# Kernel tuning notes

Measured on AMD Instinct MI355X. Metric: run time of the kernel, lower is better.

Reference implementation:

```python
import jax, jax.numpy as jnp
import numpy as np

B, L, D, H, DH, DL, NB = 8, 1024, 512, 8, 64, 64, 128
EPS = 1e-6


def layer_norm(x, g, b):
    m = jnp.mean(x, axis=-1, keepdims=True)
    v = jnp.mean((x - m) ** 2, axis=-1, keepdims=True)
    return (x - m) * jax.lax.rsqrt(v + EPS) * g + b


def rel_bias(timestamps, pos_w, ts_w):
    # position part: skew trick, pos_w has length 2L-1
    t = jnp.concatenate([pos_w, jnp.zeros((L,), pos_w.dtype)])  # (3L-1,)
    t = jnp.tile(t, L)[:-L].reshape(L, 3 * L - 2)
    rel_pos = t[:, L - 1:2 * L - 1]  # (L, L)
    # timestamp part: bucketized pairwise diffs of extended timestamps
    ext = jnp.concatenate([timestamps, timestamps[:, L - 1:L]], axis=1)  # (B, L+1)
    d = ext[:, 1:, None] - ext[:, None, :-1]  # (B, L, L)
    mag = jnp.maximum(jnp.abs(d).astype(jnp.float32), 1.0)
    bucket = jnp.clip((jnp.log(mag) / 0.301).astype(jnp.int32), 0, NB)
    rel_ts = ts_w[bucket]  # (B, L, L)
    return rel_pos[None] + rel_ts


def setup_inputs() -> dict:
    key = jax.random.key(0)
    ks = jax.random.split(key, 8)
    x = jax.random.normal(ks[0], (B, L, D), dtype=jnp.float32)
    timestamps = jnp.sort(jax.random.randint(ks[1], (B, L), 0, 1000000, dtype=jnp.int64), axis=1)
    attn_mask = jnp.triu(jnp.ones((L, L), jnp.float32), k=1)[None, None]  # 1 = masked (future)
    total_out = 2 * DL * H + 2 * DH * H
    uvqk_w = jax.random.normal(ks[2], (D, total_out), dtype=jnp.float32) * 0.02
    out_w = jax.random.normal(ks[3], (DL * H, D), dtype=jnp.float32) * 0.02
    out_b = jnp.zeros((D,), jnp.float32)
    ln1_g = jnp.ones((D,), jnp.float32); ln1_b = jnp.zeros((D,), jnp.float32)
    ln2_g = jnp.ones((DL * H,), jnp.float32); ln2_b = jnp.zeros((DL * H,), jnp.float32)
    ts_weights = jax.random.normal(ks[4], (NB + 1,), dtype=jnp.float32) * 0.02
    pos_weights = jax.random.normal(ks[5], (2 * L - 1,), dtype=jnp.float32) * 0.02
    return {"x": x, "timestamps": timestamps, "attn_mask": attn_mask,
            "uvqk_w": uvqk_w, "out_w": out_w, "out_b": out_b,
            "ln1_g": ln1_g, "ln1_b": ln1_b, "ln2_g": ln2_g, "ln2_b": ln2_b,
            "ts_weights": ts_weights, "pos_weights": pos_weights}


def reference(x, timestamps, attn_mask, uvqk_w, out_w, out_b,
              ln1_g, ln1_b, ln2_g, ln2_b, ts_weights, pos_weights):
    z = layer_norm(x, ln1_g, ln1_b)
    z = jax.nn.silu(z @ uvqk_w)  # linear_activation == 'silu'
    u, v, q, k = jnp.split(z, [DL * H, 2 * DL * H, 2 * DL * H + DH * H], axis=-1)
    q = q.reshape(B, L, H, DH)
    k = k.reshape(B, L, H, DH)
    v = v.reshape(B, L, H, DL)
    scores = jnp.einsum('bmhd,bnhd->bhmn', q, k)
    scores = scores + rel_bias(timestamps, pos_weights, ts_weights)[:, None]
    scores = jax.nn.silu(scores) / L * (1.0 - attn_mask)
    z = jnp.einsum('bhmn,bnhd->bmhd', scores, v).reshape(B, L, H * DL)
    z = layer_norm(z, ln2_g, ln2_b) * u  # gated LN
    return z @ out_w + out_b + x
```

## Files before the change

### kernel.cpp

```cpp
#include <hip/hip_runtime.h>
#include <math.h>

constexpr int Bc = 8;
constexpr int Lc = 1024;
constexpr int Dc = 512;
constexpr int Hc = 8;
constexpr int DHc = 64;
constexpr int DLc = 64;
constexpr int NBc = 128;
constexpr int TOTAL_OUT = 2 * DLc * Hc + 2 * DHc * Hc;
constexpr int ROWS = Bc * Lc;

using f32x4 = __attribute__((ext_vector_type(4))) float;
using s16x8 = __attribute__((ext_vector_type(8))) short;

__device__ __forceinline__ float bf2f(ushort u) {
    union { unsigned int i; float f; } v; v.i = ((unsigned int)u) << 16; return v.f;
}
__device__ __forceinline__ ushort f2bf(float f) {
    union { float f; unsigned int i; } v; v.f = f;
    unsigned int r = v.i + 0x7fffu + ((v.i >> 16) & 1u);
    return (ushort)(r >> 16);
}
__device__ __forceinline__ unsigned int cvtpk_bf16(float lo, float hi) {
    unsigned int r;
    asm("v_cvt_pk_bf16_f32 %0, %1, %2" : "=v"(r) : "v"(lo), "v"(hi));
    return r;
}
__device__ __forceinline__ float silu(float x) {
    float e = __expf(-x);
    return x * __builtin_amdgcn_rcpf(1.0f + e);
}

__global__ __launch_bounds__(256) void transpose_cast(const float* __restrict__ in,
                                                      ushort* __restrict__ out,
                                                      int R, int C) {
    __shared__ float tile[32][33];
    int bc = blockIdx.x * 32, br = blockIdx.y * 32;
    int tx = threadIdx.x & 31, ty = threadIdx.x >> 5;
    for (int i = ty; i < 32; i += 8) {
        int r = br + i, c = bc + tx;
        tile[i][tx] = (r < R && c < C) ? in[(size_t)r * C + c] : 0.f;
    }
    __syncthreads();
    for (int i = ty; i < 32; i += 8) {
        int c = bc + i, r = br + tx;
        if (c < C && r < R) out[(size_t)c * R + r] = f2bf(tile[tx][i]);
    }
}

__global__ __launch_bounds__(256) void ln1_kernel(const float* __restrict__ x,
                                                  const float* __restrict__ g,
                                                  const float* __restrict__ bta,
                                                  ushort* __restrict__ outp) {
    int wid = threadIdx.x >> 6, lane = threadIdx.x & 63;
    int row = blockIdx.x * 4 + wid;
    const float4* xr = (const float4*)(x + (size_t)row * Dc);
    float4 a = xr[lane * 2], c = xr[lane * 2 + 1];
    float xv[8] = {a.x, a.y, a.z, a.w, c.x, c.y, c.z, c.w};
    float s = 0.f, q = 0.f;
#pragma unroll
    for (int i = 0; i < 8; i++) { s += xv[i]; q += xv[i] * xv[i]; }
#pragma unroll
    for (int off = 32; off; off >>= 1) { s += __shfl_xor(s, off); q += __shfl_xor(q, off); }
    float mean = s * (1.f / 512.f);
    float var  = q * (1.f / 512.f) - mean * mean;
    float rstd = rsqrtf(var + 1e-6f);
    const float4* gv = (const float4*)g; const float4* bv = (const float4*)bta;
    float4 g0 = gv[lane * 2], g1 = gv[lane * 2 + 1];
    float4 b0 = bv[lane * 2], b1 = bv[lane * 2 + 1];
    float G[8] = {g0.x, g0.y, g0.z, g0.w, g1.x, g1.y, g1.z, g1.w};
    float Bv[8] = {b0.x, b0.y, b0.z, b0.w, b1.x, b1.y, b1.z, b1.w};
    union { ushort u16[8]; uint4 v; } pk;
#pragma unroll
    for (int i = 0; i < 8; i++) pk.u16[i] = f2bf((xv[i] - mean) * rstd * G[i] + Bv[i]);
    ((uint4*)(outp + (size_t)row * Dc))[lane] = pk.v;
}

__global__ __launch_bounds__(256) void bias_kernel(const int* __restrict__ ts,
                                                   const float* __restrict__ pos_w,
                                                   const float* __restrict__ ts_w,
                                                   ushort* __restrict__ biasb) {
    __shared__ float posw[2 * Lc - 1];
    __shared__ float tsw[NBc + 1];
    int tid = threadIdx.x;
    int b = blockIdx.y;
    for (int i = tid; i < 2 * Lc - 1; i += 256) posw[i] = pos_w[i];
    if (tid < NBc + 1) tsw[tid] = ts_w[tid];
    __syncthreads();
    int m = blockIdx.x * 8 + (tid >> 5);
    int n0 = (tid & 31) * 32;
    const int* tsb = ts + b * Lc;
    int mp = m + 1 < Lc ? m + 1 : Lc - 1;
    int tsm = tsb[mp];
    int pbase = (Lc - 1) + n0 - m;
    union { ushort u16[32]; uint4 v[4]; } o;
#pragma unroll
    for (int i = 0; i < 32; i += 4) {
        int4 tn = *(const int4*)&tsb[n0 + i];
        int dv[4] = {tsm - tn.x, tsm - tn.y, tsm - tn.z, tsm - tn.w};
#pragma unroll
        for (int e = 0; e < 4; e++) {
            float mag = fmaxf(fabsf((float)dv[e]), 1.f);
            int bkt = (int)(__log2f(mag) * 2.3028147f);
            bkt = bkt < 0 ? 0 : (bkt > NBc ? NBc : bkt);
            o.u16[i + e] = f2bf(posw[pbase + i + e] + tsw[bkt]);
        }
    }
    uint4* dst = (uint4*)&biasb[((size_t)b * Lc + m) * Lc + n0];
#pragma unroll
    for (int i = 0; i < 4; i++) dst[i] = o.v[i];
}

__global__ __launch_bounds__(256) void gemm1_kernel(const ushort* __restrict__ A,
                                                    const ushort* __restrict__ Bt,
                                                    ushort* __restrict__ Ub,
                                                    ushort* __restrict__ VTg,
                                                    ushort* __restrict__ Qb,
                                                    ushort* __restrict__ Kb) {
    __shared__ __align__(16) ushort As[128][72];
    __shared__ __align__(16) ushort Bs[128][72];
    int tid = threadIdx.x;
    int m0 = blockIdx.x * 128, n0 = blockIdx.y * 128;
    int w = tid >> 6, lane = tid & 63;
    int wm = (w >> 1) * 64, wn = (w & 1) * 64;
    f32x4 acc[4][4] = {};
    for (int k0 = 0; k0 < Dc; k0 += 64) {
        __syncthreads();
#pragma unroll
        for (int c = tid; c < 1024; c += 256) {
            int r = c >> 3, c8 = c & 7;
            *(uint4*)&As[r][c8 * 8] = *(const uint4*)&A[(size_t)(m0 + r) * Dc + k0 + c8 * 8];
            *(uint4*)&Bs[r][c8 * 8] = *(const uint4*)&Bt[(size_t)(n0 + r) * Dc + k0 + c8 * 8];
        }
        __syncthreads();
#pragma unroll
        for (int ks = 0; ks < 2; ++ks) {
            int kb = ks * 32 + (lane >> 4) * 8;
            s16x8 af[4], bfr[4];
#pragma unroll
            for (int i = 0; i < 4; i++) af[i] = *(const s16x8*)&As[wm + i * 16 + (lane & 15)][kb];
#pragma unroll
            for (int j = 0; j < 4; j++) bfr[j] = *(const s16x8*)&Bs[wn + j * 16 + (lane & 15)][kb];
#pragma unroll
            for (int i = 0; i < 4; i++)
#pragma unroll
                for (int j = 0; j < 4; j++)
                    acc[i][j] = __builtin_amdgcn_mfma_f32_16x16x32_bf16(af[i], bfr[j], acc[i][j], 0, 0, 0);
        }
    }
    int lr = (lane >> 4) * 4, lc = lane & 15;
#pragma unroll
    for (int i = 0; i < 4; i++)
#pragma unroll
        for (int j = 0; j < 4; j++) {
            int col = n0 + wn + j * 16 + lc;
            int sect = col >> 9, cc = col & 511;
            int row0 = m0 + wm + i * 16 + lr;
            if (sect == 1) {
                int hh = cc >> 6, dd = cc & 63;
                int bb = row0 >> 10, nn = row0 & 1023;
                ushort4 pk;
                pk.x = f2bf(silu(acc[i][j][0]));
                pk.y = f2bf(silu(acc[i][j][1]));
                pk.z = f2bf(silu(acc[i][j][2]));
                pk.w = f2bf(silu(acc[i][j][3]));
                *(ushort4*)&VTg[((size_t)((bb * 8 + hh) * 64 + dd)) * 1024 + nn] = pk;
            } else {
                ushort* dst = (sect == 0) ? Ub : (sect == 2) ? Qb : Kb;
#pragma unroll
                for (int r = 0; r < 4; r++)
                    dst[(size_t)(row0 + r) * 512 + cc] = f2bf(silu(acc[i][j][r]));
            }
        }
}

__global__ __launch_bounds__(256) void attn_kernel(const ushort* __restrict__ Qb,
                                                   const ushort* __restrict__ Kb,
                                                   const ushort* __restrict__ VTg,
                                                   const ushort* __restrict__ biasb,
                                                   ushort* __restrict__ Ob) {
    int bx = blockIdx.x;
    int h = blockIdx.y, b = blockIdx.z;
    int pidx = (bx + ((b >> 1) & 3)) & 15;
    int mt = (pidx & 1) ? (pidx >> 1) : (15 - (pidx >> 1));
    __shared__ __align__(16) ushort Ks[2][64][64];
    __shared__ __align__(16) ushort Ps[4][16][64];
    int tid = threadIdx.x, w = tid >> 6, lane = tid & 63;
    const size_t qkbase = ((size_t)b * Lc) * 512 + h * 64;
    const size_t vtbase = ((size_t)((b * 8 + h) * 64)) * 1024;
    const ushort* biasB = biasb + (size_t)b * Lc * Lc;
    const int m0 = mt * 64;
    int lc = lane & 15, g4 = lane >> 4;
    int sr = tid >> 2;
    int ss0 = (tid & 3) * 2;
    const ushort* kgrow = Kb + qkbase + (size_t)sr * 512;
    int dso0 = sr * 64 + (((ss0)     ^ (sr & 7)) * 8);
    int dso1 = sr * 64 + (((ss0 + 1) ^ (sr & 7)) * 8);

    {
        uint4 ka = *(const uint4*)(kgrow + ss0 * 8);
        uint4 kb_ = *(const uint4*)(kgrow + (ss0 + 1) * 8);
        *(uint4*)&(&Ks[0][0][0])[dso0] = ka;
        *(uint4*)&(&Ks[0][0][0])[dso1] = kb_;
    }
    __syncthreads();

    const int mrow_in64 = w * 16 + lc;
    const int mrow = m0 + mrow_in64;
    s16x8 qf[2];
#pragma unroll
    for (int ks = 0; ks < 2; ++ks)
        qf[ks] = *(const s16x8*)&Qb[qkbase + (size_t)mrow * 512 + ks * 32 + g4 * 8];

    ushort* psW = &Ps[w][0][0];
    f32x4 acc_o[4] = {};
    int ntiles = mt + 1;
    int cur = 0;
    for (int nt = 0; nt < ntiles; ++nt) {
        int n0 = nt * 64;
        s16x8 vb[2][4];
#pragma unroll
        for (int ks = 0; ks < 2; ++ks)
#pragma unroll
            for (int j = 0; j < 4; j++)
                vb[ks][j] = *(const s16x8*)&VTg[vtbase + (size_t)(j * 16 + lc) * 1024 + n0 + ks * 32 + g4 * 8];
        ushort4 bsv[4];
#pragma unroll
        for (int j = 0; j < 4; j++)
            bsv[j] = *(const ushort4*)&biasB[(size_t)mrow * Lc + n0 + j * 16 + g4 * 4];
        bool hasnext = (nt + 1 < ntiles);
        uint4 ka = {}, kb_ = {};
        if (hasnext) {
            const ushort* kgn = kgrow + (size_t)(n0 + 64) * 512;
            ka  = *(const uint4*)(kgn + ss0 * 8);
            kb_ = *(const uint4*)(kgn + (ss0 + 1) * 8);
        }
        const ushort* ksb = &Ks[cur][0][0];
        f32x4 s[4] = {};
#pragma unroll
        for (int ks = 0; ks < 2; ++ks) {
            s16x8 kf[4];
#pragma unroll
            for (int j = 0; j < 4; j++)
                kf[j] = *(const s16x8*)&ksb[(j * 16 + lc) * 64 + (((ks * 4 + g4) ^ (lc & 7)) * 8)];
#pragma unroll
            for (int j = 0; j < 4; j++)
                s[j] = __builtin_amdgcn_mfma_f32_16x16x32_bf16(kf[j], qf[ks], s[j], 0, 0, 0);
        }
        bool diag = (nt == mt);
        const ushort* bp;
#pragma unroll
        for (int j = 0; j < 4; j++) {
            float p[4];
            bp = (const ushort*)&bsv[j];
#pragma unroll
            for (int r = 0; r < 4; r++) {
                float sv = s[j][r] + bf2f(bp[r]);
                float val = silu(sv) * (1.f / (float)Lc);
                if (diag && (j * 16 + g4 * 4 + r) > mrow_in64) val = 0.f;
                p[r] = val;
            }
            unsigned int w0 = cvtpk_bf16(p[0], p[1]);
            unsigned int w1 = cvtpk_bf16(p[2], p[3]);
            int slot16 = j * 2 + (g4 >> 1);
            int off = lc * 64 + ((slot16 ^ (lc & 7)) * 8) + (g4 & 1) * 4;
            *(uint2*)&psW[off] = make_uint2(w0, w1);
        }
#pragma unroll
        for (int ks = 0; ks < 2; ++ks) {
            int rs = ks * 4 + g4;
            s16x8 pa = *(const s16x8*)&psW[lc * 64 + ((rs ^ (lc & 7)) * 8)];
#pragma unroll
            for (int j = 0; j < 4; j++)
                acc_o[j] = __builtin_amdgcn_mfma_f32_16x16x32_bf16(pa, vb[ks][j], acc_o[j], 0, 0, 0);
        }
        if (hasnext) {
            ushort* kd = &Ks[cur ^ 1][0][0];
            *(uint4*)&kd[dso0] = ka;
            *(uint4*)&kd[dso1] = kb_;
        }
        __syncthreads();
        cur ^= 1;
    }
    int mbase = m0 + w * 16 + g4 * 4;
#pragma unroll
    for (int j = 0; j < 4; j++)
#pragma unroll
        for (int r = 0; r < 4; r++) {
            int m = mbase + r;
            Ob[qkbase + (size_t)m * 512 + j * 16 + lc] = f2bf(acc_o[j][r]);
        }
}

__global__ __launch_bounds__(256) void ln2_kernel(const ushort* __restrict__ z,
                                                  const ushort* __restrict__ u,
                                                  const float* __restrict__ g,
                                                  const float* __restrict__ bta,
                                                  ushort* __restrict__ outp) {
    int wid = threadIdx.x >> 6, lane = threadIdx.x & 63;
    int row = blockIdx.x * 4 + wid;
    uint4 zv = ((const uint4*)(z + (size_t)row * 512))[lane];
    ushort* zu = (ushort*)&zv;
    float xv[8], s = 0.f, q = 0.f;
#pragma unroll
    for (int i = 0; i < 8; i++) { xv[i] = bf2f(zu[i]); s += xv[i]; q += xv[i] * xv[i]; }
#pragma unroll
    for (int off = 32; off; off >>= 1) { s += __shfl_xor(s, off); q += __shfl_xor(q, off); }
    float mean = s * (1.f / 512.f);
    float var  = q * (1.f / 512.f) - mean * mean;
    float rstd = rsqrtf(var + 1e-6f);
    uint4 uv = ((const uint4*)(u + (size_t)row * 512))[lane];
    ushort* uu = (ushort*)&uv;
    const float4* gv = (const float4*)g; const float4* bv = (const float4*)bta;
    float4 g0 = gv[lane * 2], g1 = gv[lane * 2 + 1];
    float4 b0 = bv[lane * 2], b1 = bv[lane * 2 + 1];
    float G[8] = {g0.x, g0.y, g0.z, g0.w, g1.x, g1.y, g1.z, g1.w};
    float Bv[8] = {b0.x, b0.y, b0.z, b0.w, b1.x, b1.y, b1.z, b1.w};
    union { ushort u16[8]; uint4 v; } pk;
#pragma unroll
    for (int i = 0; i < 8; i++)
        pk.u16[i] = f2bf(((xv[i] - mean) * rstd * G[i] + Bv[i]) * bf2f(uu[i]));
    ((uint4*)(outp + (size_t)row * 512))[lane] = pk.v;
}

__global__ __launch_bounds__(256) void gemm2_kernel(const ushort* __restrict__ A,
                                                    const ushort* __restrict__ Bt,
                                                    const float* __restrict__ ob,
                                                    const float* __restrict__ x,
                                                    float* __restrict__ outp) {
    __shared__ __align__(16) ushort As[128][72];
    __shared__ __align__(16) ushort Bs[128][72];
    int tid = threadIdx.x;
    int m0 = blockIdx.x * 128, n0 = blockIdx.y * 128;
    int w = tid >> 6, lane = tid & 63;
    int wm = (w >> 1) * 64, wn = (w & 1) * 64;
    f32x4 acc[4][4] = {};
    for (int k0 = 0; k0 < Dc; k0 += 64) {
        __syncthreads();
#pragma unroll
        for (int c = tid; c < 1024; c += 256) {
            int r = c >> 3, c8 = c & 7;
            *(uint4*)&As[r][c8 * 8] = *(const uint4*)&A[(size_t)(m0 + r) * Dc + k0 + c8 * 8];
            *(uint4*)&Bs[r][c8 * 8] = *(const uint4*)&Bt[(size_t)(n0 + r) * Dc + k0 + c8 * 8];
        }
        __syncthreads();
#pragma unroll
        for (int ks = 0; ks < 2; ++ks) {
            int kb = ks * 32 + (lane >> 4) * 8;
            s16x8 af[4], bfr[4];
#pragma unroll
            for (int i = 0; i < 4; i++) af[i] = *(const s16x8*)&As[wm + i * 16 + (lane & 15)][kb];
#pragma unroll
            for (int j = 0; j < 4; j++) bfr[j] = *(const s16x8*)&Bs[wn + j * 16 + (lane & 15)][kb];
#pragma unroll
            for (int i = 0; i < 4; i++)
#pragma unroll
                for (int j = 0; j < 4; j++)
                    acc[i][j] = __builtin_amdgcn_mfma_f32_16x16x32_bf16(af[i], bfr[j], acc[i][j], 0, 0, 0);
        }
    }
    int lr = (lane >> 4) * 4, lc = lane & 15;
#pragma unroll
    for (int i = 0; i < 4; i++)
#pragma unroll
        for (int j = 0; j < 4; j++) {
            int col = n0 + wn + j * 16 + lc;
            float bias = ob[col];
#pragma unroll
            for (int r = 0; r < 4; r++) {
                int row = m0 + wm + i * 16 + lr + r;
                size_t off = (size_t)row * 512 + col;
                outp[off] = acc[i][j][r] + bias + x[off];
            }
        }
}

extern "C" void kernel_launch(void* const* d_in, const int* in_sizes, int n_in,
                              void* d_out, int out_size, void* d_ws, size_t ws_size,
                              hipStream_t stream) {
    const float* x      = (const float*)d_in[0];
    const int*   tsp    = (const int*)d_in[1];
    const float* uvqk_w = (const float*)d_in[3];
    const float* out_w  = (const float*)d_in[4];
    const float* out_b  = (const float*)d_in[5];
    const float* ln1_g  = (const float*)d_in[6];
    const float* ln1_b  = (const float*)d_in[7];
    const float* ln2_g  = (const float*)d_in[8];
    const float* ln2_b  = (const float*)d_in[9];
    const float* ts_w   = (const float*)d_in[10];
    const float* pos_w  = (const float*)d_in[11];
    float* outp = (float*)d_out;

    char* ws = (char*)d_ws;
    size_t off = 0;
    auto alloc = [&](size_t bytes) { char* p = ws + off; off += (bytes + 255) & ~(size_t)255; return p; };
    const size_t MAT = (size_t)ROWS * 512 * sizeof(ushort);
    ushort* W1T = (ushort*)alloc((size_t)TOTAL_OUT * Dc * 2);
    ushort* W2T = (ushort*)alloc((size_t)Dc * Dc * 2);
    ushort* X1  = (ushort*)alloc(MAT);
    ushort* Ub  = (ushort*)alloc(MAT);
    ushort* VTg = (ushort*)alloc(MAT);
    ushort* Qb  = (ushort*)alloc(MAT);
    ushort* Kb  = (ushort*)alloc(MAT);
    ushort* Ob  = (ushort*)alloc(MAT);
    ushort* BIAS = (ushort*)alloc((size_t)Bc * Lc * Lc * 2);
    ushort* A2  = X1;

    transpose_cast<<<dim3(TOTAL_OUT / 32, Dc / 32), 256, 0, stream>>>(uvqk_w, W1T, Dc, TOTAL_OUT);
    transpose_cast<<<dim3(Dc / 32, Dc / 32), 256, 0, stream>>>(out_w, W2T, Dc, Dc);
    bias_kernel<<<dim3(Lc / 8, Bc), 256, 0, stream>>>(tsp, pos_w, ts_w, BIAS);
    ln1_kernel<<<ROWS / 4, 256, 0, stream>>>(x, ln1_g, ln1_b, X1);
    gemm1_kernel<<<dim3(ROWS / 128, TOTAL_OUT / 128), 256, 0, stream>>>(X1, W1T, Ub, VTg, Qb, Kb);
    attn_kernel<<<dim3(16, Hc, Bc), 256, 0, stream>>>(Qb, Kb, VTg, BIAS, Ob);
    ln2_kernel<<<ROWS / 4, 256, 0, stream>>>(Ob, Ub, ln2_g, ln2_b, A2);
    gemm2_kernel<<<dim3(ROWS / 128, Dc / 128), 256, 0, stream>>>(A2, W2T, out_b, x, outp);
}
```

Measured before the change: 246.4 us.

## Pair causal query tiles per attention block and transpose GEMM epilogues for vector stores

The attention kernel now gives each block two complementary query tiles (i and 15-i), so every block does the same amount of causal work. The two tiles share each loaded K tile and V fragment, and the grid shrinks to half as many blocks. Both GEMMs swap the MFMA operand order so each lane holds four consecutive columns. That lets the U/Q/K and final-output epilogues use packed vector stores, while the VT epilogue now uses scalar stores. The change trades fewer blocks and higher register pressure for balanced work and more K/V reuse.

```diff
diff --git a/kernel.cpp b/kernel.cpp
--- a/kernel.cpp
+++ b/kernel.cpp
@@ -146,33 +146,35 @@
             for (int i = 0; i < 4; i++)
 #pragma unroll
                 for (int j = 0; j < 4; j++)
-                    acc[i][j] = __builtin_amdgcn_mfma_f32_16x16x32_bf16(af[i], bfr[j], acc[i][j], 0, 0, 0);
+                    acc[i][j] = __builtin_amdgcn_mfma_f32_16x16x32_bf16(bfr[j], af[i], acc[i][j], 0, 0, 0);
         }
     }
     int lr = (lane >> 4) * 4, lc = lane & 15;
 #pragma unroll
-    for (int i = 0; i < 4; i++)
+    for (int i = 0; i < 4; i++) {
+        int m = m0 + wm + i * 16 + lc;
 #pragma unroll
         for (int j = 0; j < 4; j++) {
-            int col = n0 + wn + j * 16 + lc;
-            int sect = col >> 9, cc = col & 511;
-            int row0 = m0 + wm + i * 16 + lr;
+            int col0 = n0 + wn + j * 16 + lr;
+            int sect = col0 >> 9, cc0 = col0 & 511;
             if (sect == 1) {
-                int hh = cc >> 6, dd = cc & 63;
-                int bb = row0 >> 10, nn = row0 & 1023;
+                int hh = cc0 >> 6, dd0 = cc0 & 63;
+                int bb = m >> 10, nn = m & 1023;
+                size_t base = ((size_t)((bb * 8 + hh) * 64 + dd0)) * 1024 + nn;
+#pragma unroll
+                for (int r = 0; r < 4; r++)
+                    VTg[base + (size_t)r * 1024] = f2bf(silu(acc[i][j][r]));
+            } else {
+                ushort* dst = (sect == 0) ? Ub : (sect == 2) ? Qb : Kb;
                 ushort4 pk;
                 pk.x = f2bf(silu(acc[i][j][0]));
                 pk.y = f2bf(silu(acc[i][j][1]));
                 pk.z = f2bf(silu(acc[i][j][2]));
                 pk.w = f2bf(silu(acc[i][j][3]));
-                *(ushort4*)&VTg[((size_t)((bb * 8 + hh) * 64 + dd)) * 1024 + nn] = pk;
-            } else {
-                ushort* dst = (sect == 0) ? Ub : (sect == 2) ? Qb : Kb;
-#pragma unroll
-                for (int r = 0; r < 4; r++)
-                    dst[(size_t)(row0 + r) * 512 + cc] = f2bf(silu(acc[i][j][r]));
+                *(ushort4*)&dst[(size_t)m * 512 + cc0] = pk;
             }
         }
+    }
 }
 
 __global__ __launch_bounds__(256) void attn_kernel(const ushort* __restrict__ Qb,
@@ -180,17 +182,15 @@
                                                    const ushort* __restrict__ VTg,
                                                    const ushort* __restrict__ biasb,
                                                    ushort* __restrict__ Ob) {
-    int bx = blockIdx.x;
+    int iA = blockIdx.x;
+    int iB = 15 - iA;
     int h = blockIdx.y, b = blockIdx.z;
-    int pidx = (bx + ((b >> 1) & 3)) & 15;
-    int mt = (pidx & 1) ? (pidx >> 1) : (15 - (pidx >> 1));
     __shared__ __align__(16) ushort Ks[2][64][64];
-    __shared__ __align__(16) ushort Ps[4][16][64];
+    __shared__ __align__(16) ushort Ps[4][2][16][64];
     int tid = threadIdx.x, w = tid >> 6, lane = tid & 63;
     const size_t qkbase = ((size_t)b * Lc) * 512 + h * 64;
     const size_t vtbase = ((size_t)((b * 8 + h) * 64)) * 1024;
-    const ushort* biasB = biasb + (size_t)b * Lc * Lc;
-    const int m0 = mt * 64;
+    const ushort* biasT = biasb + (size_t)b * Lc * Lc;
     int lc = lane & 15, g4 = lane >> 4;
     int sr = tid >> 2;
     int ss0 = (tid & 3) * 2;
@@ -206,30 +206,38 @@
     }
     __syncthreads();
 
-    const int mrow_in64 = w * 16 + lc;
-    const int mrow = m0 + mrow_in64;
-    s16x8 qf[2];
-#pragma unroll
-    for (int ks = 0; ks < 2; ++ks)
-        qf[ks] = *(const s16x8*)&Qb[qkbase + (size_t)mrow * 512 + ks * 32 + g4 * 8];
-
-    ushort* psW = &Ps[w][0][0];
-    f32x4 acc_o[4] = {};
-    int ntiles = mt + 1;
+    const int m0A = iA * 64, m0B = iB * 64;
+    const int mloc = w * 16 + lc;
+    const int mrowA = m0A + mloc, mrowB = m0B + mloc;
+    s16x8 qfA[2], qfB[2];
+#pragma unroll
+    for (int ks = 0; ks < 2; ++ks) {
+        qfA[ks] = *(const s16x8*)&Qb[qkbase + (size_t)mrowA * 512 + ks * 32 + g4 * 8];
+        qfB[ks] = *(const s16x8*)&Qb[qkbase + (size_t)mrowB * 512 + ks * 32 + g4 * 8];
+    }
+    ushort* psA = &Ps[w][0][0][0];
+    ushort* psB = &Ps[w][1][0][0];
+    f32x4 accA[4] = {}, accB[4] = {};
     int cur = 0;
-    for (int nt = 0; nt < ntiles; ++nt) {
+    for (int nt = 0; nt <= iB; ++nt) {
         int n0 = nt * 64;
+        bool aact = (nt <= iA);
         s16x8 vb[2][4];
 #pragma unroll
         for (int ks = 0; ks < 2; ++ks)
 #pragma unroll
             for (int j = 0; j < 4; j++)
                 vb[ks][j] = *(const s16x8*)&VTg[vtbase + (size_t)(j * 16 + lc) * 1024 + n0 + ks * 32 + g4 * 8];
-        ushort4 bsv[4];
+        ushort4 bsvB[4], bsvA[4];
 #pragma unroll
         for (int j = 0; j < 4; j++)
-            bsv[j] = *(const ushort4*)&biasB[(size_t)mrow * Lc + n0 + j * 16 + g4 * 4];
-        bool hasnext = (nt + 1 < ntiles);
+            bsvB[j] = *(const ushort4*)&biasT[(size_t)mrowB * Lc + n0 + j * 16 + g4 * 4];
+        if (aact) {
+#pragma unroll
+            for (int j = 0; j < 4; j++)
+                bsvA[j] = *(const ushort4*)&biasT[(size_t)mrowA * Lc + n0 + j * 16 + g4 * 4];
+        }
+        bool hasnext = (nt < iB);
         uint4 ka = {}, kb_ = {};
         if (hasnext) {
             const ushort* kgn = kgrow + (size_t)(n0 + 64) * 512;
@@ -237,7 +245,7 @@
             kb_ = *(const uint4*)(kgn + (ss0 + 1) * 8);
         }
         const ushort* ksb = &Ks[cur][0][0];
-        f32x4 s[4] = {};
+        f32x4 sB[4] = {}, sA[4] = {};
 #pragma unroll
         for (int ks = 0; ks < 2; ++ks) {
             s16x8 kf[4];
@@ -245,35 +253,65 @@
             for (int j = 0; j < 4; j++)
                 kf[j] = *(const s16x8*)&ksb[(j * 16 + lc) * 64 + (((ks * 4 + g4) ^ (lc & 7)) * 8)];
 #pragma unroll
-            for (int j = 0; j < 4; j++)
-                s[j] = __builtin_amdgcn_mfma_f32_16x16x32_bf16(kf[j], qf[ks], s[j], 0, 0, 0);
-        }
-        bool diag = (nt == mt);
-        const ushort* bp;
-#pragma unroll
-        for (int j = 0; j < 4; j++) {
-            float p[4];
-            bp = (const ushort*)&bsv[j];
-#pragma unroll
-            for (int r = 0; r < 4; r++) {
-                float sv = s[j][r] + bf2f(bp[r]);
-                float val = silu(sv) * (1.f / (float)Lc);
-                if (diag && (j * 16 + g4 * 4 + r) > mrow_in64) val = 0.f;
-                p[r] = val;
+            for (int j = 0; j < 4; j++) {
+                sB[j] = __builtin_amdgcn_mfma_f32_16x16x32_bf16(kf[j], qfB[ks], sB[j], 0, 0, 0);
+                if (aact)
+                    sA[j] = __builtin_amdgcn_mfma_f32_16x16x32_bf16(kf[j], qfA[ks], sA[j], 0, 0, 0);
             }
-            unsigned int w0 = cvtpk_bf16(p[0], p[1]);
-            unsigned int w1 = cvtpk_bf16(p[2], p[3]);
-            int slot16 = j * 2 + (g4 >> 1);
-            int off = lc * 64 + ((slot16 ^ (lc & 7)) * 8) + (g4 & 1) * 4;
-            *(uint2*)&psW[off] = make_uint2(w0, w1);
+        }
+        {
+            bool diag = (nt == iB);
+#pragma unroll
+            for (int j = 0; j < 4; j++) {
+                const ushort* bp = (const ushort*)&bsvB[j];
+                float p[4];
+#pragma unroll
+                for (int r = 0; r < 4; r++) {
+                    float sv = sB[j][r] + bf2f(bp[r]);
+                    float val = silu(sv) * (1.f / (float)Lc);
+                    if (diag && (j * 16 + g4 * 4 + r) > mloc) val = 0.f;
+                    p[r] = val;
+                }
+                unsigned int w0 = cvtpk_bf16(p[0], p[1]);
+                unsigned int w1 = cvtpk_bf16(p[2], p[3]);
+                int slot16 = j * 2 + (g4 >> 1);
+                int off = lc * 64 + ((slot16 ^ (lc & 7)) * 8) + (g4 & 1) * 4;
+                *(uint2*)&psB[off] = make_uint2(w0, w1);
+            }
+        }
+        if (aact) {
+            bool diag = (nt == iA);
+#pragma unroll
+            for (int j = 0; j < 4; j++) {
+                const ushort* bp = (const ushort*)&bsvA[j];
+                float p[4];
+#pragma unroll
+                for (int r = 0; r < 4; r++) {
+                    float sv = sA[j][r] + bf2f(bp[r]);
+                    float val = silu(sv) * (1.f / (float)Lc);
+                    if (diag && (j * 16 + g4 * 4 + r) > mloc) val = 0.f;
+                    p[r] = val;
+                }
+                unsigned int w0 = cvtpk_bf16(p[0], p[1]);
+                unsigned int w1 = cvtpk_bf16(p[2], p[3]);
+                int slot16 = j * 2 + (g4 >> 1);
+                int off = lc * 64 + ((slot16 ^ (lc & 7)) * 8) + (g4 & 1) * 4;
+                *(uint2*)&psA[off] = make_uint2(w0, w1);
+            }
         }
 #pragma unroll
         for (int ks = 0; ks < 2; ++ks) {
             int rs = ks * 4 + g4;
-            s16x8 pa = *(const s16x8*)&psW[lc * 64 + ((rs ^ (lc & 7)) * 8)];
+            s16x8 paB = *(const s16x8*)&psB[lc * 64 + ((rs ^ (lc & 7)) * 8)];
 #pragma unroll
             for (int j = 0; j < 4; j++)
-                acc_o[j] = __builtin_amdgcn_mfma_f32_16x16x32_bf16(pa, vb[ks][j], acc_o[j], 0, 0, 0);
+                accB[j] = __builtin_amdgcn_mfma_f32_16x16x32_bf16(paB, vb[ks][j], accB[j], 0, 0, 0);
+            if (aact) {
+                s16x8 paA = *(const s16x8*)&psA[lc * 64 + ((rs ^ (lc & 7)) * 8)];
+#pragma unroll
+                for (int j = 0; j < 4; j++)
+                    accA[j] = __builtin_amdgcn_mfma_f32_16x16x32_bf16(paA, vb[ks][j], accA[j], 0, 0, 0);
+            }
         }
         if (hasnext) {
             ushort* kd = &Ks[cur ^ 1][0][0];
@@ -283,13 +321,14 @@
         __syncthreads();
         cur ^= 1;
     }
-    int mbase = m0 + w * 16 + g4 * 4;
+    int mbA = m0A + w * 16 + g4 * 4;
+    int mbB = m0B + w * 16 + g4 * 4;
 #pragma unroll
     for (int j = 0; j < 4; j++)
 #pragma unroll
         for (int r = 0; r < 4; r++) {
-            int m = mbase + r;
-            Ob[qkbase + (size_t)m * 512 + j * 16 + lc] = f2bf(acc_o[j][r]);
+            Ob[qkbase + (size_t)(mbA + r) * 512 + j * 16 + lc] = f2bf(accA[j][r]);
+            Ob[qkbase + (size_t)(mbB + r) * 512 + j * 16 + lc] = f2bf(accB[j][r]);
         }
 }
 
@@ -357,23 +396,27 @@
             for (int i = 0; i < 4; i++)
 #pragma unroll
                 for (int j = 0; j < 4; j++)
-                    acc[i][j] = __builtin_amdgcn_mfma_f32_16x16x32_bf16(af[i], bfr[j], acc[i][j], 0, 0, 0);
+                    acc[i][j] = __builtin_amdgcn_mfma_f32_16x16x32_bf16(bfr[j], af[i], acc[i][j], 0, 0, 0);
         }
     }
     int lr = (lane >> 4) * 4, lc = lane & 15;
 #pragma unroll
-    for (int i = 0; i < 4; i++)
+    for (int i = 0; i < 4; i++) {
+        int m = m0 + wm + i * 16 + lc;
 #pragma unroll
         for (int j = 0; j < 4; j++) {
-            int col = n0 + wn + j * 16 + lc;
-            float bias = ob[col];
-#pragma unroll
-            for (int r = 0; r < 4; r++) {
-                int row = m0 + wm + i * 16 + lr + r;
-                size_t off = (size_t)row * 512 + col;
-                outp[off] = acc[i][j][r] + bias + x[off];
-            }
-        }
+            int col0 = n0 + wn + j * 16 + lr;
+            size_t off = (size_t)m * 512 + col0;
+            float4 xb = *(const float4*)&x[off];
+            float4 obv = *(const float4*)&ob[col0];
+            float4 o;
+            o.x = acc[i][j][0] + obv.x + xb.x;
+            o.y = acc[i][j][1] + obv.y + xb.y;
+            o.z = acc[i][j][2] + obv.z + xb.z;
+            o.w = acc[i][j][3] + obv.w + xb.w;
+            *(float4*)&outp[off] = o;
+        }
+    }
 }
 
 extern "C" void kernel_launch(void* const* d_in, const int* in_sizes, int n_in,
@@ -412,7 +455,7 @@
     bias_kernel<<<dim3(Lc / 8, Bc), 256, 0, stream>>>(tsp, pos_w, ts_w, BIAS);
     ln1_kernel<<<ROWS / 4, 256, 0, stream>>>(x, ln1_g, ln1_b, X1);
     gemm1_kernel<<<dim3(ROWS / 128, TOTAL_OUT / 128), 256, 0, stream>>>(X1, W1T, Ub, VTg, Qb, Kb);
-    attn_kernel<<<dim3(16, Hc, Bc), 256, 0, stream>>>(Qb, Kb, VTg, BIAS, Ob);
+    attn_kernel<<<dim3(8, Hc, Bc), 256, 0, stream>>>(Qb, Kb, VTg, BIAS, Ob);
     ln2_kernel<<<ROWS / 4, 256, 0, stream>>>(Ob, Ub, ln2_g, ln2_b, A2);
     gemm2_kernel<<<dim3(ROWS / 128, Dc / 128), 256, 0, stream>>>(A2, W2T, out_b, x, outp);
 }
```

Result: no change. 245.8 us (-0.2%).
